# Performance work log

Hardware: AMD Instinct MI355X
Metric: run time of the kernel (lower is better)

The kernel has to match this reference:

```python
import jax, jax.numpy as jnp
import numpy as np

LN_EPS = 1e-5


def _ln_all_nonbatch(t):
    # torch nn.LayerNorm(t.size()[1:]) created fresh each call: identity affine,
    # normalize jointly over all non-batch dims, biased variance, eps=1e-5.
    axes = tuple(range(1, t.ndim))
    mu = jnp.mean(t, axis=axes, keepdims=True)
    var = jnp.mean(jnp.square(t - mu), axis=axes, keepdims=True)
    return (t - mu) / jnp.sqrt(var + LN_EPS)


def setup_inputs() -> dict:
    key = jax.random.key(0)
    kx, kq, kk, kv = jax.random.split(key, 4)
    B, S, E, d = 32, 1024, 768, 64
    x = jax.random.normal(kx, (B, S, E), dtype=jnp.float32)
    Wq = jax.random.normal(kq, (E, d), dtype=jnp.float32)
    Wk = jax.random.normal(kk, (E, d), dtype=jnp.float32)
    Wv = jax.random.normal(kv, (E, d), dtype=jnp.float32)
    return {"x": x, "Wq": Wq, "Wk": Wk, "Wv": Wv}


def reference(x, Wq, Wk, Wv):
    # x: [B,S,E]; Wq/Wk/Wv: [E,d]
    Q = jnp.einsum('bse,ed->bsd', x, Wq)            # [B,S,d]
    K = jnp.swapaxes(jnp.einsum('bse,ed->bsd', x, Wk), -2, -1)  # [B,d,S]
    V = jnp.einsum('bse,ed->bsd', x, Wv)            # [B,S,d]
    Q = _ln_all_nonbatch(Q)
    K = _ln_all_nonbatch(K)
    V = _ln_all_nonbatch(V)
    d = Q.shape[-1]  # K.shape[1] after transpose == head dim
    scores = jnp.einsum('bsd,bdt->bst', Q, K) / jnp.sqrt(jnp.float32(d))  # [B,S,S]
    attn = jax.nn.softmax(scores, axis=-1)
    return jnp.einsum('bst,btd->bsd', attn, V)      # [B,S,d]
```

## Files before the change

### kernel.cpp

```cpp
#include <hip/hip_runtime.h>
#include <hip/hip_fp16.h>

typedef _Float16 f16x8 __attribute__((ext_vector_type(8)));
typedef _Float16 f16x4 __attribute__((ext_vector_type(4)));
typedef float    f32x4 __attribute__((ext_vector_type(4)));

#define NB   32
#define SEQ  1024
#define EDIM 768
#define HD   64
#define MTOT (NB * SEQ)

__global__ __launch_bounds__(256) void pack_w(const float* __restrict__ Wq,
                                              const float* __restrict__ Wk,
                                              const float* __restrict__ Wv,
                                              _Float16* __restrict__ Wt) {
    int c = blockIdx.x;
    const float* src = (c < 64) ? Wq : (c < 128) ? Wk : Wv;
    int cc = c & 63;
    for (int e = threadIdx.x; e < EDIM; e += 256)
        Wt[(size_t)c * EDIM + e] = (_Float16)src[(size_t)e * HD + cc];
}

__global__ __launch_bounds__(256) void proj_kernel(const float* __restrict__ x,
                                                   const _Float16* __restrict__ Wt,
                                                   _Float16* __restrict__ q16,
                                                   _Float16* __restrict__ k16,
                                                   _Float16* __restrict__ v16,
                                                   float* __restrict__ part,
                                                   float* __restrict__ ksum) {
    __shared__ _Float16 xs[2][64][72];
    __shared__ _Float16 wsh[2][192][72];
    __shared__ float red[4][6];
    const int tid  = threadIdx.x;
    const int wave = tid >> 6, lane = tid & 63;
    const int lr = lane & 15, lk = (lane >> 4) * 8, lrow = (lane >> 4) * 4;
    const int m0 = blockIdx.x * 64;

    f32x4 acc[12] = {};
    f32x4 xv[4];
    f16x8 wv[6];

    #pragma unroll
    for (int i = 0; i < 4; ++i) {
        int lin = tid + i * 256, r = lin >> 4, c4 = (lin & 15) * 4;
        xv[i] = *(const f32x4*)&x[(size_t)(m0 + r) * EDIM + c4];
    }
    #pragma unroll
    for (int i = 0; i < 6; ++i) {
        int lin = tid + i * 256, c = lin >> 3, c8 = (lin & 7) * 8;
        wv[i] = *(const f16x8*)&Wt[(size_t)c * EDIM + c8];
    }
    #pragma unroll
    for (int i = 0; i < 4; ++i) {
        int lin = tid + i * 256, r = lin >> 4, c4 = (lin & 15) * 4;
        f16x4 h;
        h[0] = (_Float16)xv[i][0]; h[1] = (_Float16)xv[i][1];
        h[2] = (_Float16)xv[i][2]; h[3] = (_Float16)xv[i][3];
        *(f16x4*)&xs[0][r][c4] = h;
    }
    #pragma unroll
    for (int i = 0; i < 6; ++i) {
        int lin = tid + i * 256, c = lin >> 3, c8 = (lin & 7) * 8;
        *(f16x8*)&wsh[0][c][c8] = wv[i];
    }
    __syncthreads();

    for (int kt = 0; kt < 12; ++kt) {
        const int cur = kt & 1;
        if (kt < 11) {
            const int e0 = (kt + 1) * 64;
            #pragma unroll
            for (int i = 0; i < 4; ++i) {
                int lin = tid + i * 256, r = lin >> 4, c4 = (lin & 15) * 4;
                xv[i] = *(const f32x4*)&x[(size_t)(m0 + r) * EDIM + e0 + c4];
            }
            #pragma unroll
            for (int i = 0; i < 6; ++i) {
                int lin = tid + i * 256, c = lin >> 3, c8 = (lin & 7) * 8;
                wv[i] = *(const f16x8*)&Wt[(size_t)c * EDIM + e0 + c8];
            }
        }
        f16x8 a0  = *(const f16x8*)&xs[cur][wave * 16 + lr][lk];
        f16x8 a0b = *(const f16x8*)&xs[cur][wave * 16 + lr][32 + lk];
        #pragma unroll
        for (int nb = 0; nb < 12; ++nb) {
            f16x8 b0 = *(const f16x8*)&wsh[cur][nb * 16 + lr][lk];
            f16x8 b1 = *(const f16x8*)&wsh[cur][nb * 16 + lr][32 + lk];
            acc[nb] = __builtin_amdgcn_mfma_f32_16x16x32_f16(a0,  b0, acc[nb], 0, 0, 0);
            acc[nb] = __builtin_amdgcn_mfma_f32_16x16x32_f16(a0b, b1, acc[nb], 0, 0, 0);
        }
        if (kt < 11) {
            #pragma unroll
            for (int i = 0; i < 4; ++i) {
                int lin = tid + i * 256, r = lin >> 4, c4 = (lin & 15) * 4;
                f16x4 h;
                h[0] = (_Float16)xv[i][0]; h[1] = (_Float16)xv[i][1];
                h[2] = (_Float16)xv[i][2]; h[3] = (_Float16)xv[i][3];
                *(f16x4*)&xs[cur ^ 1][r][c4] = h;
            }
            #pragma unroll
            for (int i = 0; i < 6; ++i) {
                int lin = tid + i * 256, c = lin >> 3, c8 = (lin & 7) * 8;
                *(f16x8*)&wsh[cur ^ 1][c][c8] = wv[i];
            }
            __syncthreads();
        }
    }

    #pragma unroll
    for (int nb = 0; nb < 12; ++nb) {
        _Float16* dst = (nb < 4) ? q16 : (nb < 8) ? k16 : v16;
        int lc = (nb & 3) * 16 + lr;
        #pragma unroll
        for (int j = 0; j < 4; ++j)
            dst[(size_t)(m0 + wave * 16 + lrow + j) * HD + lc] = (_Float16)acc[nb][j];
    }

    #pragma unroll
    for (int j = 0; j < 4; ++j) {
        float ks = (acc[4][j] + acc[5][j]) + (acc[6][j] + acc[7][j]);
        ks += __shfl_xor(ks, 1); ks += __shfl_xor(ks, 2);
        ks += __shfl_xor(ks, 4); ks += __shfl_xor(ks, 8);
        if (lr == 0) ksum[m0 + wave * 16 + lrow + j] = ks;
    }

    #pragma unroll
    for (int t3 = 0; t3 < 3; ++t3) {
        float s = 0.f, q = 0.f;
        #pragma unroll
        for (int nb = t3 * 4; nb < t3 * 4 + 4; ++nb)
            #pragma unroll
            for (int j = 0; j < 4; ++j) { float v = acc[nb][j]; s += v; q += v * v; }
        #pragma unroll
        for (int off = 1; off < 64; off <<= 1) {
            s += __shfl_xor(s, off); q += __shfl_xor(q, off);
        }
        if (lane == 0) { red[wave][t3 * 2] = s; red[wave][t3 * 2 + 1] = q; }
    }
    __syncthreads();
    if (tid < 6)
        part[blockIdx.x * 6 + tid] = red[0][tid] + red[1][tid] + red[2][tid] + red[3][tid];
}

__global__ __launch_bounds__(64) void stats_reduce(const float* __restrict__ part,
                                                   float* __restrict__ stats) {
    int b = blockIdx.x, a = threadIdx.x;
    if (a < 3) {
        double s = 0.0, q = 0.0;
        for (int i = 0; i < 16; ++i) {
            s += (double)part[(b * 16 + i) * 6 + a * 2];
            q += (double)part[(b * 16 + i) * 6 + a * 2 + 1];
        }
        double mean = s / 65536.0;
        double var  = q / 65536.0 - mean * mean;
        stats[b * 8 + a * 2 + 0] = (float)mean;
        stats[b * 8 + a * 2 + 1] = (float)(1.0 / sqrt(var + 1e-5));
    }
}

__global__ __launch_bounds__(256) void transpose_v(const _Float16* __restrict__ v16,
                                                   _Float16* __restrict__ v16t) {
    __shared__ _Float16 t[64][72];
    int b = blockIdx.x >> 4, s0 = (blockIdx.x & 15) * 64;
    int tid = threadIdx.x;
    for (int i = 0; i < 2; ++i) {
        int lin = tid + i * 256;
        int s = lin >> 3, d8 = (lin & 7) * 8;
        *(f16x8*)&t[s][d8] = *(const f16x8*)&v16[((size_t)b * SEQ + s0 + s) * HD + d8];
    }
    __syncthreads();
    for (int i = 0; i < 2; ++i) {
        int lin = tid + i * 256;
        int d = lin >> 3, s8 = (lin & 7) * 8;
        f16x8 g;
        for (int k = 0; k < 8; ++k) g[k] = t[s8 + k][d];
        *(f16x8*)&v16t[((size_t)b * HD + d) * SEQ + s0 + s8] = g;
    }
}

__global__ __launch_bounds__(256) void attn_kernel(const _Float16* __restrict__ q16,
                                                   const _Float16* __restrict__ k16,
                                                   const _Float16* __restrict__ v16t,
                                                   const float* __restrict__ stats,
                                                   const float* __restrict__ ksum,
                                                   float* __restrict__ out) {
    __shared__ _Float16 ksm[64][72];
    __shared__ _Float16 vsm[64][72];
    __shared__ _Float16 psm[4][16][72];
    const int d_ = blockIdx.x;
    const int b = (d_ & 7) * 4 + ((d_ >> 3) & 3), qt = d_ >> 5;
    const int tid = threadIdx.x, wave = tid >> 6, lane = tid & 63;
    const int lr = lane & 15, lk = (lane >> 4) * 8, lrow = (lane >> 4) * 4;
    const float sscale = stats[b * 8 + 1] * stats[b * 8 + 3] * 0.125f;
    const float adjscale = sscale * stats[b * 8 + 0];
    const float mv = stats[b * 8 + 4], rv = stats[b * 8 + 5];
    const int q0 = qt * 64 + wave * 16;
    const _Float16* Qb = q16 + ((size_t)b * SEQ + q0) * HD;
    const float* ksb = ksum + b * SEQ;

    f16x8 aq0 = *(const f16x8*)&Qb[(size_t)lr * HD + lk];
    f16x8 aq1 = *(const f16x8*)&Qb[(size_t)lr * HD + 32 + lk];

    f32x4 o[4] = {};
    float mrow[4], lsum[4];
    for (int j = 0; j < 4; ++j) { mrow[j] = -1e30f; lsum[j] = 0.f; }

    for (int kv0 = 0; kv0 < SEQ; kv0 += 64) {
        for (int i = 0; i < 2; ++i) {
            int lin = tid + i * 256;
            int r = lin >> 3, c = (lin & 7) * 8;
            *(f16x8*)&ksm[r][c] = *(const f16x8*)&k16[((size_t)b * SEQ + kv0 + r) * HD + c];
        }
        for (int i = 0; i < 2; ++i) {
            int lin = tid + i * 256;
            int dd = lin >> 3, c = (lin & 7) * 8;
            *(f16x8*)&vsm[dd][c] = *(const f16x8*)&v16t[((size_t)b * HD + dd) * SEQ + kv0 + c];
        }
        __syncthreads();

        f32x4 sa[4];
        float adjv[4];
        for (int cb = 0; cb < 4; ++cb) {
            sa[cb] = (f32x4){0.f, 0.f, 0.f, 0.f};
            f16x8 bk0 = *(const f16x8*)&ksm[cb * 16 + lr][lk];
            f16x8 bk1 = *(const f16x8*)&ksm[cb * 16 + lr][32 + lk];
            sa[cb] = __builtin_amdgcn_mfma_f32_16x16x32_f16(aq0, bk0, sa[cb], 0, 0, 0);
            sa[cb] = __builtin_amdgcn_mfma_f32_16x16x32_f16(aq1, bk1, sa[cb], 0, 0, 0);
            adjv[cb] = adjscale * ksb[kv0 + cb * 16 + lr];
        }

        for (int j = 0; j < 4; ++j) {
            float sv0 = sa[0][j] * sscale - adjv[0];
            float sv1 = sa[1][j] * sscale - adjv[1];
            float sv2 = sa[2][j] * sscale - adjv[2];
            float sv3 = sa[3][j] * sscale - adjv[3];
            float pm = fmaxf(fmaxf(sv0, sv1), fmaxf(sv2, sv3));
            pm = fmaxf(pm, __shfl_xor(pm, 1));
            pm = fmaxf(pm, __shfl_xor(pm, 2));
            pm = fmaxf(pm, __shfl_xor(pm, 4));
            pm = fmaxf(pm, __shfl_xor(pm, 8));
            float mnew  = fmaxf(mrow[j], pm);
            float alpha = __expf(mrow[j] - mnew);
            mrow[j] = mnew;
            float p0 = __expf(sv0 - mnew), p1 = __expf(sv1 - mnew);
            float p2 = __expf(sv2 - mnew), p3 = __expf(sv3 - mnew);
            sa[0][j] = p0; sa[1][j] = p1; sa[2][j] = p2; sa[3][j] = p3;
            float rs = (p0 + p1) + (p2 + p3);
            rs += __shfl_xor(rs, 1); rs += __shfl_xor(rs, 2);
            rs += __shfl_xor(rs, 4); rs += __shfl_xor(rs, 8);
            lsum[j] = lsum[j] * alpha + rs;
            o[0][j] *= alpha; o[1][j] *= alpha; o[2][j] *= alpha; o[3][j] *= alpha;
        }
        for (int cb = 0; cb < 4; ++cb)
            for (int j = 0; j < 4; ++j)
                psm[wave][lrow + j][cb * 16 + lr] = (_Float16)sa[cb][j];

        f16x8 pa0 = *(const f16x8*)&psm[wave][lr][lk];
        f16x8 pa1 = *(const f16x8*)&psm[wave][lr][32 + lk];
        for (int db = 0; db < 4; ++db) {
            f16x8 bv0 = *(const f16x8*)&vsm[db * 16 + lr][lk];
            f16x8 bv1 = *(const f16x8*)&vsm[db * 16 + lr][32 + lk];
            o[db] = __builtin_amdgcn_mfma_f32_16x16x32_f16(pa0, bv0, o[db], 0, 0, 0);
            o[db] = __builtin_amdgcn_mfma_f32_16x16x32_f16(pa1, bv1, o[db], 0, 0, 0);
        }
        __syncthreads();
    }

    for (int j = 0; j < 4; ++j) {
        float inv = 1.f / lsum[j];
        size_t row = (size_t)b * SEQ + q0 + lrow + j;
        for (int db = 0; db < 4; ++db)
            out[row * HD + db * 16 + lr] = rv * (o[db][j] * inv - mv);
    }
}

extern "C" void kernel_launch(void* const* d_in, const int* in_sizes, int n_in,
                              void* d_out, int out_size, void* d_ws, size_t ws_size,
                              hipStream_t stream) {
    const float* x  = (const float*)d_in[0];
    const float* Wq = (const float*)d_in[1];
    const float* Wk = (const float*)d_in[2];
    const float* Wv = (const float*)d_in[3];
    float* out = (float*)d_out;
    char* ws = (char*)d_ws;

    _Float16* Wt   = (_Float16*)ws;
    float* stats   = (float*)(ws + 0x50000);
    float* ksum    = (float*)(ws + 0x51000);
    float* part    = (float*)(ws + 0x72000);
    _Float16* q16  = (_Float16*)(ws + 0x100000);
    _Float16* k16  = (_Float16*)(ws + 0x500000);
    _Float16* v16  = (_Float16*)(ws + 0x900000);
    _Float16* v16t = (_Float16*)(ws + 0xD00000);

    pack_w<<<192, 256, 0, stream>>>(Wq, Wk, Wv, Wt);
    proj_kernel<<<MTOT / 64, 256, 0, stream>>>(x, Wt, q16, k16, v16, part, ksum);
    stats_reduce<<<NB, 64, 0, stream>>>(part, stats);
    transpose_v<<<NB * 16, 256, 0, stream>>>(v16, v16t);
    attn_kernel<<<NB * 16, 256, 0, stream>>>(q16, k16, v16t, stats, ksum, out);
}
```

Baseline: 77.21 us.

## Fuse V transpose into projection, repartition MFMA work by column, use exp2

The projection kernel now splits its 192 output columns across waves, with each wave covering all 64 rows, instead of splitting by rows. This lets the V tile be written directly in transposed layout, so the separate transpose_v kernel and its extra global round trip are removed. K row sums and the LN statistics are now reduced through shared memory across waves. The attention kernel folds log2(e) into the score scale, uses exp2f instead of __expf, and adds unroll pragmas. The transposed V stores are 8-byte strided writes, which may coalesce less well than before.

```diff
diff --git a/kernel.cpp b/kernel.cpp
--- a/kernel.cpp
+++ b/kernel.cpp
@@ -10,6 +10,7 @@
 #define EDIM 768
 #define HD   64
 #define MTOT (NB * SEQ)
+#define LOG2E 1.44269504088896340736f
 
 __global__ __launch_bounds__(256) void pack_w(const float* __restrict__ Wq,
                                               const float* __restrict__ Wk,
@@ -26,18 +27,19 @@
                                                    const _Float16* __restrict__ Wt,
                                                    _Float16* __restrict__ q16,
                                                    _Float16* __restrict__ k16,
-                                                   _Float16* __restrict__ v16,
+                                                   _Float16* __restrict__ v16t,
                                                    float* __restrict__ part,
                                                    float* __restrict__ ksum) {
     __shared__ _Float16 xs[2][64][72];
     __shared__ _Float16 wsh[2][192][72];
     __shared__ float red[4][6];
-    const int tid  = threadIdx.x;
-    const int wave = tid >> 6, lane = tid & 63;
+    __shared__ float kred[2][64];
+    const int tid = threadIdx.x, wave = tid >> 6, lane = tid & 63;
     const int lr = lane & 15, lk = (lane >> 4) * 8, lrow = (lane >> 4) * 4;
     const int m0 = blockIdx.x * 64;
-
-    f32x4 acc[12] = {};
+    const int bb = m0 >> 10;
+
+    f32x4 acc[4][3] = {};
     f32x4 xv[4];
     f16x8 wv[6];
 
@@ -81,14 +83,22 @@
                 wv[i] = *(const f16x8*)&Wt[(size_t)c * EDIM + e0 + c8];
             }
         }
-        f16x8 a0  = *(const f16x8*)&xs[cur][wave * 16 + lr][lk];
-        f16x8 a0b = *(const f16x8*)&xs[cur][wave * 16 + lr][32 + lk];
-        #pragma unroll
-        for (int nb = 0; nb < 12; ++nb) {
+        f16x8 af[4][2];
+        #pragma unroll
+        for (int rg = 0; rg < 4; ++rg) {
+            af[rg][0] = *(const f16x8*)&xs[cur][rg * 16 + lr][lk];
+            af[rg][1] = *(const f16x8*)&xs[cur][rg * 16 + lr][32 + lk];
+        }
+        #pragma unroll
+        for (int c = 0; c < 3; ++c) {
+            const int nb = wave * 3 + c;
             f16x8 b0 = *(const f16x8*)&wsh[cur][nb * 16 + lr][lk];
             f16x8 b1 = *(const f16x8*)&wsh[cur][nb * 16 + lr][32 + lk];
-            acc[nb] = __builtin_amdgcn_mfma_f32_16x16x32_f16(a0,  b0, acc[nb], 0, 0, 0);
-            acc[nb] = __builtin_amdgcn_mfma_f32_16x16x32_f16(a0b, b1, acc[nb], 0, 0, 0);
+            #pragma unroll
+            for (int rg = 0; rg < 4; ++rg) {
+                acc[rg][c] = __builtin_amdgcn_mfma_f32_16x16x32_f16(af[rg][0], b0, acc[rg][c], 0, 0, 0);
+                acc[rg][c] = __builtin_amdgcn_mfma_f32_16x16x32_f16(af[rg][1], b1, acc[rg][c], 0, 0, 0);
+            }
         }
         if (kt < 11) {
             #pragma unroll
@@ -109,36 +119,68 @@
     }
 
     #pragma unroll
-    for (int nb = 0; nb < 12; ++nb) {
-        _Float16* dst = (nb < 4) ? q16 : (nb < 8) ? k16 : v16;
-        int lc = (nb & 3) * 16 + lr;
-        #pragma unroll
-        for (int j = 0; j < 4; ++j)
-            dst[(size_t)(m0 + wave * 16 + lrow + j) * HD + lc] = (_Float16)acc[nb][j];
-    }
-
-    #pragma unroll
-    for (int j = 0; j < 4; ++j) {
-        float ks = (acc[4][j] + acc[5][j]) + (acc[6][j] + acc[7][j]);
-        ks += __shfl_xor(ks, 1); ks += __shfl_xor(ks, 2);
-        ks += __shfl_xor(ks, 4); ks += __shfl_xor(ks, 8);
-        if (lr == 0) ksum[m0 + wave * 16 + lrow + j] = ks;
-    }
-
-    #pragma unroll
-    for (int t3 = 0; t3 < 3; ++t3) {
+    for (int rg = 0; rg < 4; ++rg) {
+        const int rbase = m0 + rg * 16 + lrow;
+        const int rowin = (m0 & 1023) + rg * 16 + lrow;
+        #pragma unroll
+        for (int c = 0; c < 3; ++c) {
+            const int nb = wave * 3 + c;
+            if (nb < 8) {
+                _Float16* dst = (nb < 4) ? q16 : k16;
+                int lc = (nb & 3) * 16 + lr;
+                #pragma unroll
+                for (int j = 0; j < 4; ++j)
+                    dst[(size_t)(rbase + j) * HD + lc] = (_Float16)acc[rg][c][j];
+            } else {
+                int col = (nb & 3) * 16 + lr;
+                f16x4 h;
+                #pragma unroll
+                for (int j = 0; j < 4; ++j) h[j] = (_Float16)acc[rg][c][j];
+                *(f16x4*)&v16t[((size_t)(bb * 64 + col)) * SEQ + rowin] = h;
+            }
+        }
+    }
+
+    if (wave == 1 || wave == 2) {
+        #pragma unroll
+        for (int rg = 0; rg < 4; ++rg) {
+            #pragma unroll
+            for (int j = 0; j < 4; ++j) {
+                float ks = (wave == 1) ? (acc[rg][1][j] + acc[rg][2][j])
+                                       : (acc[rg][0][j] + acc[rg][1][j]);
+                ks += __shfl_xor(ks, 1); ks += __shfl_xor(ks, 2);
+                ks += __shfl_xor(ks, 4); ks += __shfl_xor(ks, 8);
+                if (lr == 0) kred[wave - 1][rg * 16 + lrow + j] = ks;
+            }
+        }
+    }
+
+    float sq = 0.f, qq = 0.f, sk = 0.f, qk = 0.f, sv = 0.f, qv = 0.f;
+    #pragma unroll
+    for (int c = 0; c < 3; ++c) {
+        const int nb = wave * 3 + c;
         float s = 0.f, q = 0.f;
         #pragma unroll
-        for (int nb = t3 * 4; nb < t3 * 4 + 4; ++nb)
-            #pragma unroll
-            for (int j = 0; j < 4; ++j) { float v = acc[nb][j]; s += v; q += v * v; }
-        #pragma unroll
-        for (int off = 1; off < 64; off <<= 1) {
-            s += __shfl_xor(s, off); q += __shfl_xor(q, off);
-        }
-        if (lane == 0) { red[wave][t3 * 2] = s; red[wave][t3 * 2 + 1] = q; }
+        for (int rg = 0; rg < 4; ++rg)
+            #pragma unroll
+            for (int j = 0; j < 4; ++j) { float v = acc[rg][c][j]; s += v; q += v * v; }
+        if (nb < 4)      { sq += s; qq += q; }
+        else if (nb < 8) { sk += s; qk += q; }
+        else             { sv += s; qv += q; }
+    }
+    #pragma unroll
+    for (int off = 1; off < 64; off <<= 1) {
+        sq += __shfl_xor(sq, off); qq += __shfl_xor(qq, off);
+        sk += __shfl_xor(sk, off); qk += __shfl_xor(qk, off);
+        sv += __shfl_xor(sv, off); qv += __shfl_xor(qv, off);
+    }
+    if (lane == 0) {
+        red[wave][0] = sq; red[wave][1] = qq;
+        red[wave][2] = sk; red[wave][3] = qk;
+        red[wave][4] = sv; red[wave][5] = qv;
     }
     __syncthreads();
+    if (tid < 64) ksum[m0 + tid] = kred[0][tid] + kred[1][tid];
     if (tid < 6)
         part[blockIdx.x * 6 + tid] = red[0][tid] + red[1][tid] + red[2][tid] + red[3][tid];
 }
@@ -156,26 +198,6 @@
         double var  = q / 65536.0 - mean * mean;
         stats[b * 8 + a * 2 + 0] = (float)mean;
         stats[b * 8 + a * 2 + 1] = (float)(1.0 / sqrt(var + 1e-5));
-    }
-}
-
-__global__ __launch_bounds__(256) void transpose_v(const _Float16* __restrict__ v16,
-                                                   _Float16* __restrict__ v16t) {
-    __shared__ _Float16 t[64][72];
-    int b = blockIdx.x >> 4, s0 = (blockIdx.x & 15) * 64;
-    int tid = threadIdx.x;
-    for (int i = 0; i < 2; ++i) {
-        int lin = tid + i * 256;
-        int s = lin >> 3, d8 = (lin & 7) * 8;
-        *(f16x8*)&t[s][d8] = *(const f16x8*)&v16[((size_t)b * SEQ + s0 + s) * HD + d8];
-    }
-    __syncthreads();
-    for (int i = 0; i < 2; ++i) {
-        int lin = tid + i * 256;
-        int d = lin >> 3, s8 = (lin & 7) * 8;
-        f16x8 g;
-        for (int k = 0; k < 8; ++k) g[k] = t[s8 + k][d];
-        *(f16x8*)&v16t[((size_t)b * HD + d) * SEQ + s0 + s8] = g;
     }
 }
 
@@ -192,7 +214,7 @@
     const int b = (d_ & 7) * 4 + ((d_ >> 3) & 3), qt = d_ >> 5;
     const int tid = threadIdx.x, wave = tid >> 6, lane = tid & 63;
     const int lr = lane & 15, lk = (lane >> 4) * 8, lrow = (lane >> 4) * 4;
-    const float sscale = stats[b * 8 + 1] * stats[b * 8 + 3] * 0.125f;
+    const float sscale = stats[b * 8 + 1] * stats[b * 8 + 3] * 0.125f * LOG2E;
     const float adjscale = sscale * stats[b * 8 + 0];
     const float mv = stats[b * 8 + 4], rv = stats[b * 8 + 5];
     const int q0 = qt * 64 + wave * 16;
@@ -204,6 +226,7 @@
 
     f32x4 o[4] = {};
     float mrow[4], lsum[4];
+    #pragma unroll
     for (int j = 0; j < 4; ++j) { mrow[j] = -1e30f; lsum[j] = 0.f; }
 
     for (int kv0 = 0; kv0 < SEQ; kv0 += 64) {
@@ -221,6 +244,7 @@
 
         f32x4 sa[4];
         float adjv[4];
+        #pragma unroll
         for (int cb = 0; cb < 4; ++cb) {
             sa[cb] = (f32x4){0.f, 0.f, 0.f, 0.f};
             f16x8 bk0 = *(const f16x8*)&ksm[cb * 16 + lr][lk];
@@ -230,6 +254,7 @@
             adjv[cb] = adjscale * ksb[kv0 + cb * 16 + lr];
         }
 
+        #pragma unroll
         for (int j = 0; j < 4; ++j) {
             float sv0 = sa[0][j] * sscale - adjv[0];
             float sv1 = sa[1][j] * sscale - adjv[1];
@@ -241,10 +266,10 @@
             pm = fmaxf(pm, __shfl_xor(pm, 4));
             pm = fmaxf(pm, __shfl_xor(pm, 8));
             float mnew  = fmaxf(mrow[j], pm);
-            float alpha = __expf(mrow[j] - mnew);
+            float alpha = exp2f(mrow[j] - mnew);
             mrow[j] = mnew;
-            float p0 = __expf(sv0 - mnew), p1 = __expf(sv1 - mnew);
-            float p2 = __expf(sv2 - mnew), p3 = __expf(sv3 - mnew);
+            float p0 = exp2f(sv0 - mnew), p1 = exp2f(sv1 - mnew);
+            float p2 = exp2f(sv2 - mnew), p3 = exp2f(sv3 - mnew);
             sa[0][j] = p0; sa[1][j] = p1; sa[2][j] = p2; sa[3][j] = p3;
             float rs = (p0 + p1) + (p2 + p3);
             rs += __shfl_xor(rs, 1); rs += __shfl_xor(rs, 2);
@@ -252,12 +277,15 @@
             lsum[j] = lsum[j] * alpha + rs;
             o[0][j] *= alpha; o[1][j] *= alpha; o[2][j] *= alpha; o[3][j] *= alpha;
         }
+        #pragma unroll
         for (int cb = 0; cb < 4; ++cb)
+            #pragma unroll
             for (int j = 0; j < 4; ++j)
                 psm[wave][lrow + j][cb * 16 + lr] = (_Float16)sa[cb][j];
 
         f16x8 pa0 = *(const f16x8*)&psm[wave][lr][lk];
         f16x8 pa1 = *(const f16x8*)&psm[wave][lr][32 + lk];
+        #pragma unroll
         for (int db = 0; db < 4; ++db) {
             f16x8 bv0 = *(const f16x8*)&vsm[db * 16 + lr][lk];
             f16x8 bv1 = *(const f16x8*)&vsm[db * 16 + lr][32 + lk];
@@ -267,9 +295,11 @@
         __syncthreads();
     }
 
+    #pragma unroll
     for (int j = 0; j < 4; ++j) {
         float inv = 1.f / lsum[j];
         size_t row = (size_t)b * SEQ + q0 + lrow + j;
+        #pragma unroll
         for (int db = 0; db < 4; ++db)
             out[row * HD + db * 16 + lr] = rv * (o[db][j] * inv - mv);
     }
@@ -291,12 +321,10 @@
     float* part    = (float*)(ws + 0x72000);
     _Float16* q16  = (_Float16*)(ws + 0x100000);
     _Float16* k16  = (_Float16*)(ws + 0x500000);
-    _Float16* v16  = (_Float16*)(ws + 0x900000);
-    _Float16* v16t = (_Float16*)(ws + 0xD00000);
+    _Float16* v16t = (_Float16*)(ws + 0x900000);
 
     pack_w<<<192, 256, 0, stream>>>(Wq, Wk, Wv, Wt);
-    proj_kernel<<<MTOT / 64, 256, 0, stream>>>(x, Wt, q16, k16, v16, part, ksum);
+    proj_kernel<<<MTOT / 64, 256, 0, stream>>>(x, Wt, q16, k16, v16t, part, ksum);
     stats_reduce<<<NB, 64, 0, stream>>>(part, stats);
-    transpose_v<<<NB * 16, 256, 0, stream>>>(v16, v16t);
     attn_kernel<<<NB * 16, 256, 0, stream>>>(q16, k16, v16t, stats, ksum, out);
 }
```

Measured after the change: 76.43 us. Within noise of the previous version (-1.0%).
